# Optimization experiments

Measured on AMD Instinct MI355X. Metric: run time of the kernel, lower is better.

The kernel has to match this reference:

```python
import jax, jax.numpy as jnp
import numpy as np

N = 50000          # nodes
E = 800000         # edges per metapath
P = 4              # metapaths
IN = 256           # in_size
D = 32 * 8         # out_size * layer_num_heads = 256
SEM_H = 128        # SemanticAttention hidden


def setup_inputs() -> dict:
    key = jax.random.key(0)
    ks = jax.random.split(key, 8)
    h = jax.random.normal(ks[0], (N, IN), dtype=jnp.float32)
    src = jax.random.randint(ks[1], (P, E), 0, N, dtype=jnp.int32)
    dst = jax.random.randint(ks[2], (P, E), 0, N, dtype=jnp.int32)
    # per-metapath GraphConv weights (Glorot-ish scale)
    W_gc = jax.random.normal(ks[3], (P, IN, D), dtype=jnp.float32) / np.sqrt(IN)
    b_gc = jnp.zeros((P, D), dtype=jnp.float32)
    # SemanticAttention: Linear(D, SEM_H) -> tanh -> Linear(SEM_H, 1, bias=False)
    W1 = jax.random.normal(ks[4], (D, SEM_H), dtype=jnp.float32) / np.sqrt(D)
    b1 = jnp.zeros((SEM_H,), dtype=jnp.float32)
    w2 = jax.random.normal(ks[5], (SEM_H,), dtype=jnp.float32) / np.sqrt(SEM_H)
    return {"h": h, "src": src, "dst": dst, "W_gc": W_gc, "b_gc": b_gc,
            "W1": W1, "b1": b1, "w2": w2}


def _graph_conv(h, src, dst, W, b):
    # DGL GraphConv with norm='both': D_dst^{-1/2} A D_src^{-1/2} (h W) + b
    ones = jnp.ones((src.shape[0],), dtype=h.dtype)
    deg_out = jnp.clip(jax.ops.segment_sum(ones, src, num_segments=N), 1.0)
    deg_in = jnp.clip(jax.ops.segment_sum(ones, dst, num_segments=N), 1.0)
    x = (h @ W) * jax.lax.rsqrt(deg_out)[:, None]          # [N, D]
    agg = jax.ops.segment_sum(x[src], dst, num_segments=N)  # gather-scatter [N, D]
    return agg * jax.lax.rsqrt(deg_in)[:, None] + b


def reference(h, src, dst, W_gc, b_gc, W1, b1, w2):
    # per-metapath GraphConv (fixed small loop over P metapaths)
    zs = [_graph_conv(h, src[p], dst[p], W_gc[p], b_gc[p]) for p in range(P)]
    z = jnp.stack(zs, axis=1)                               # [N, P, D]
    # SemanticAttention: project -> mean over nodes -> softmax over metapaths
    s = jnp.tanh(z @ W1 + b1) @ w2                          # [N, P]
    beta = jax.nn.softmax(s.mean(axis=0), axis=0)           # [P]
    return jnp.einsum('npd,p->nd', z, beta)                 # [N, D]
```

## Files before the change

### kernel.cpp

```cpp
#include <hip/hip_runtime.h>

#define NN 50000
#define NE 800000
#define NP 4
#define DIN 256
#define DD 256
#define NH 128
#define SA 40
#define NSEG 16
#define SEGE (NE / NSEG)
#define HCH 16384
#define NHC 4
#define SCH 8192
#define NSC 7
#define SPAD(k) ((k) + ((k) >> 5))

typedef __attribute__((ext_vector_type(8))) short bf16x8;
typedef __attribute__((ext_vector_type(4))) float f32x4;
typedef __attribute__((ext_vector_type(2))) float f32x2;

__device__ __forceinline__ unsigned short f2bf(float f) {
  unsigned u = __float_as_uint(f);
  u += 0x7fff + ((u >> 16) & 1);
  return (unsigned short)(u >> 16);
}
__device__ __forceinline__ float bfl(unsigned u) { return __uint_as_float(u << 16); }
__device__ __forceinline__ float bfh(unsigned u) { return __uint_as_float(u & 0xffff0000u); }


__global__ __launch_bounds__(256) void hist2d_kernel(const int* __restrict__ idx,
                                                     int* __restrict__ cnt) {
  int bx = blockIdx.x;
  int c = bx % NHC, s = bx / NHC;
  int p = blockIdx.y;
  int base = c * HCH, nk = min(HCH, NN - base);
  __shared__ int hs[HCH];
  for (int k = threadIdx.x; k < HCH; k += 256) hs[k] = 0;
  __syncthreads();
  const int4* a4 = (const int4*)(idx + (size_t)p * NE + (size_t)s * SEGE);
  for (int i = threadIdx.x; i < SEGE / 4; i += 256) {
    int4 v = a4[i];
    int k;
    k = v.x - base; if ((unsigned)k < (unsigned)nk) atomicAdd(&hs[k], 1);
    k = v.y - base; if ((unsigned)k < (unsigned)nk) atomicAdd(&hs[k], 1);
    k = v.z - base; if ((unsigned)k < (unsigned)nk) atomicAdd(&hs[k], 1);
    k = v.w - base; if ((unsigned)k < (unsigned)nk) atomicAdd(&hs[k], 1);
  }
  __syncthreads();
  int* out = cnt + (size_t)(p * NSEG + s) * NN + base;
  for (int k = threadIdx.x; k < nk; k += 256) out[k] = hs[k];
}


__global__ __launch_bounds__(1024) void scanA_kernel(
    int* __restrict__ cntD, const int* __restrict__ cntS,
    float* __restrict__ rin, float* __restrict__ rout,
    int* __restrict__ row_ptr, int* __restrict__ chunkdeg) {
  int c = blockIdx.x, p = blockIdx.y;
  int base = c * SCH, nk = min(SCH, NN - base);
  __shared__ int sdeg[SCH + (SCH >> 5)];
  __shared__ int wtot[16], wexc[16];
  int t = threadIdx.x;
  for (int kk = t; kk < SCH; kk += 1024) {
    int run = 0;
    if (kk < nk) {
      size_t o = (size_t)(p * NSEG) * NN + base + kk;
      for (int s = 0; s < NSEG; ++s) {
        size_t oo = o + (size_t)s * NN;
        int v = cntD[oo];
        cntD[oo] = run;
        run += v;
      }
      rin[(size_t)p * NN + base + kk] = rsqrtf((float)max(run, 1));
      int rs = 0;
      for (int s = 0; s < NSEG; ++s) rs += cntS[o + (size_t)s * NN];
      rout[(size_t)p * NN + base + kk] = rsqrtf((float)max(rs, 1));
    }
    sdeg[SPAD(kk)] = run;
  }
  __syncthreads();
  int loc[8];
  int ssum = 0;
#pragma unroll
  for (int j = 0; j < 8; ++j) { loc[j] = ssum; ssum += sdeg[SPAD(t * 8 + j)]; }
  int incl = ssum;
  int lane = t & 63, w = t >> 6;
#pragma unroll
  for (int o = 1; o < 64; o <<= 1) {
    int v = __shfl_up(incl, o);
    if (lane >= o) incl += v;
  }
  if (lane == 63) wtot[w] = incl;
  __syncthreads();
  if (t == 0) {
    int r = 0;
    for (int i = 0; i < 16; ++i) { wexc[i] = r; r += wtot[i]; }
  }
  __syncthreads();
  int tbase = wexc[w] + incl - ssum;
  int* rp = row_ptr + (size_t)p * (NN + 1) + base;
#pragma unroll
  for (int j = 0; j < 8; ++j) {
    int k = t * 8 + j;
    if (k < nk) rp[k] = tbase + loc[j];
  }
  if (t == 1023) chunkdeg[p * NSC + c] = tbase + ssum;
}


__global__ void scanB_kernel(const int* __restrict__ chunkdeg, int* __restrict__ chunk_base,
                             int* __restrict__ row_ptr) {
  int t = threadIdx.x;
  if (t < NP) {
    int run = 0;
    for (int c = 0; c < NSC; ++c) { chunk_base[t * NSC + c] = run; run += chunkdeg[t * NSC + c]; }
    row_ptr[(size_t)t * (NN + 1) + NN] = NE;
  }
}

__global__ __launch_bounds__(1024) void rpfin_kernel(int* __restrict__ row_ptr,
                                                     const int* __restrict__ chunk_base) {
  int k = blockIdx.x * 1024 + threadIdx.x, p = blockIdx.y;
  if (k < NN) row_ptr[(size_t)p * (NN + 1) + k] += chunk_base[p * NSC + (k >> 13)];
}


__global__ __launch_bounds__(256) void scatter_kernel(
    const int* __restrict__ src, const int* __restrict__ dst,
    const int* __restrict__ cntD, const int* __restrict__ row_ptr, int* __restrict__ col) {
  int bx = blockIdx.x;
  int c = bx % NHC, s = bx / NHC;
  int p = blockIdx.y;
  int base = c * HCH, nk = min(HCH, NN - base);
  __shared__ int cur[HCH];
  for (int k = threadIdx.x; k < nk; k += 256)
    cur[k] = row_ptr[(size_t)p * (NN + 1) + base + k] +
             cntD[(size_t)(p * NSEG + s) * NN + base + k];
  __syncthreads();
  const int4* d4 = (const int4*)(dst + (size_t)p * NE + (size_t)s * SEGE);
  const int4* s4 = (const int4*)(src + (size_t)p * NE + (size_t)s * SEGE);
  int* colp = col + (size_t)p * NE;
  for (int i = threadIdx.x; i < SEGE / 4; i += 256) {
    int4 dv = d4[i];
    int4 sv = s4[i];
    int k;
    k = dv.x - base; if ((unsigned)k < (unsigned)nk) colp[atomicAdd(&cur[k], 1)] = sv.x;
    k = dv.y - base; if ((unsigned)k < (unsigned)nk) colp[atomicAdd(&cur[k], 1)] = sv.y;
    k = dv.z - base; if ((unsigned)k < (unsigned)nk) colp[atomicAdd(&cur[k], 1)] = sv.z;
    k = dv.w - base; if ((unsigned)k < (unsigned)nk) colp[atomicAdd(&cur[k], 1)] = sv.w;
  }
}


__global__ void cvt_h_kernel(const float4* __restrict__ h4, ushort4* __restrict__ h2) {
  int i = blockIdx.x * blockDim.x + threadIdx.x;
  if (i >= NN * DIN / 4) return;
  float4 v = h4[i];
  ushort4 o;
  o.x = f2bf(v.x); o.y = f2bf(v.y); o.z = f2bf(v.z); o.w = f2bf(v.w);
  h2[i] = o;
}


__global__ __launch_bounds__(256) void agg_kernel(
    const ushort* __restrict__ h2, const int* __restrict__ col,
    const int* __restrict__ row_ptr, const float* __restrict__ rout,
    const float* __restrict__ rin, ushort* __restrict__ g) {
  __shared__ int2 sW[4][64];
  int p = blockIdx.y;
  int v = blockIdx.x * 4 + (threadIdx.x >> 6);
  int lane = threadIdx.x & 63;
  int wv = threadIdx.x >> 6;
  const int* colp = col + (size_t)p * NE;
  const float* rop = rout + (size_t)p * NN;
  int beg = row_ptr[p * (NN + 1) + v], end = row_ptr[p * (NN + 1) + v + 1];
  const char* hb = (const char*)h2 + (size_t)lane * 8;
  f32x2 accA0 = {0.f, 0.f}, accA1 = {0.f, 0.f};
  f32x2 accB0 = {0.f, 0.f}, accB1 = {0.f, 0.f};
  for (int j0 = beg; j0 < end; j0 += 64) {
    int nw = end - j0;
    if (nw > 64) nw = 64;
    int cv = 0;
    float rv = 0.f;
    if (lane < nw) { cv = colp[j0 + lane]; rv = rop[cv]; }
    sW[wv][lane] = make_int2(cv, __float_as_int(rv));
    int nwb = (nw + 7) & ~7;
    for (int t = 0; t < nwb; t += 8) {
      int2 w[8];
#pragma unroll
      for (int q = 0; q < 8; ++q) w[q] = sW[wv][t + q];
      uint2 u[8];
#pragma unroll
      for (int q = 0; q < 8; ++q)
        u[q] = *(const uint2*)(hb + ((size_t)(unsigned)w[q].x << 9));
#pragma unroll
      for (int q = 0; q < 8; ++q) {
        float r = __int_as_float(w[q].y);
        f32x2 rr = {r, r};
        if (q & 1) {
          asm("v_pk_fma_f32 %0, %1, %2, %0" : "+v"(accB0) : "v"(rr), "v"((f32x2){bfl(u[q].x), bfh(u[q].x)}));
          asm("v_pk_fma_f32 %0, %1, %2, %0" : "+v"(accB1) : "v"(rr), "v"((f32x2){bfl(u[q].y), bfh(u[q].y)}));
        } else {
          asm("v_pk_fma_f32 %0, %1, %2, %0" : "+v"(accA0) : "v"(rr), "v"((f32x2){bfl(u[q].x), bfh(u[q].x)}));
          asm("v_pk_fma_f32 %0, %1, %2, %0" : "+v"(accA1) : "v"(rr), "v"((f32x2){bfl(u[q].y), bfh(u[q].y)}));
        }
      }
    }
  }
  float ri = rin[(size_t)p * NN + v];
  f32x2 s0 = accA0 + accB0;
  f32x2 s1 = accA1 + accB1;
  ushort4 o;
  o.x = f2bf(s0.x * ri); o.y = f2bf(s0.y * ri);
  o.z = f2bf(s1.x * ri); o.w = f2bf(s1.y * ri);
  ((ushort4*)(g + ((size_t)p * NN + v) * DIN))[lane] = o;
}


__global__ void wmulcvec_kernel(const float* __restrict__ Wgc, const float* __restrict__ bgc,
                                const float* __restrict__ W1, const float* __restrict__ b1,
                                ushort* __restrict__ Mt, float* __restrict__ cvec) {
  int p = blockIdx.y, k = blockIdx.x, j = threadIdx.x;
  if (k < DIN) {
    const float* wrow = Wgc + ((size_t)p * DIN + k) * DD;
    float s = 0.f;
    for (int d = 0; d < DD; ++d) s = fmaf(wrow[d], W1[(size_t)d * NH + j], s);
    Mt[((size_t)p * NH + j) * DIN + k] = f2bf(s);
  } else {
    const float* b = bgc + (size_t)p * DD;
    float s = b1[j];
    for (int d = 0; d < DD; ++d) s = fmaf(b[d], W1[(size_t)d * NH + j], s);
    cvec[p * NH + j] = s;
  }
}


__global__ __launch_bounds__(256) void gemm_sem(
    const ushort* __restrict__ g, const ushort* __restrict__ Mt,
    const float* __restrict__ cvec, const float* __restrict__ w2,
    float* __restrict__ ssum) {
  __shared__ ushort As[128 * SA];
  __shared__ ushort Bs[128 * SA];
  __shared__ float wsumf[4];
  const int tid = threadIdx.x;
  const int p = blockIdx.y;
  const int row0 = blockIdx.x * 128;
  const int wave = tid >> 6, lane = tid & 63;
  const int wr = wave >> 1, wc = wave & 1;
  const int srow = tid >> 2, sseg = tid & 3;
  const int fr = lane & 15, fk = (lane >> 4) * 8;
  const ushort* Ag = g + (size_t)p * NN * DIN;
  const ushort* Bg = Mt + (size_t)p * NH * DIN;
  int ar0 = row0 + srow; if (ar0 >= NN) ar0 = NN - 1;
  int ar1 = row0 + srow + 64; if (ar1 >= NN) ar1 = NN - 1;
  f32x4 acc[4][4] = {};
  for (int k2 = 0; k2 < DIN; k2 += 32) {
    uint4 av0 = *(const uint4*)(Ag + (size_t)ar0 * DIN + k2 + sseg * 8);
    uint4 av1 = *(const uint4*)(Ag + (size_t)ar1 * DIN + k2 + sseg * 8);
    uint4 bv0 = *(const uint4*)(Bg + (size_t)srow * DIN + k2 + sseg * 8);
    uint4 bv1 = *(const uint4*)(Bg + (size_t)(srow + 64) * DIN + k2 + sseg * 8);
    __syncthreads();
    *(uint4*)&As[srow * SA + sseg * 8] = av0;
    *(uint4*)&As[(srow + 64) * SA + sseg * 8] = av1;
    *(uint4*)&Bs[srow * SA + sseg * 8] = bv0;
    *(uint4*)&Bs[(srow + 64) * SA + sseg * 8] = bv1;
    __syncthreads();
    bf16x8 af[4], bfv[4];
#pragma unroll
    for (int t = 0; t < 4; ++t) {
      af[t] = *(const bf16x8*)&As[(wr * 64 + t * 16 + fr) * SA + fk];
      bfv[t] = *(const bf16x8*)&Bs[(wc * 64 + t * 16 + fr) * SA + fk];
    }
#pragma unroll
    for (int mt = 0; mt < 4; ++mt)
#pragma unroll
      for (int nt = 0; nt < 4; ++nt)
        acc[mt][nt] = __builtin_amdgcn_mfma_f32_16x16x32_bf16(af[mt], bfv[nt], acc[mt][nt], 0, 0, 0);
  }
  float s = 0.f;
#pragma unroll
  for (int nt = 0; nt < 4; ++nt) {
    int c = wc * 64 + nt * 16 + fr;
    float cc = cvec[p * NH + c];
    float ww = w2[c];
#pragma unroll
    for (int mt = 0; mt < 4; ++mt)
#pragma unroll
      for (int i = 0; i < 4; ++i) {
        int r = row0 + wr * 64 + mt * 16 + (lane >> 4) * 4 + i;
        if (r < NN) {
          float x = acc[mt][nt][i] + cc;
          x = fminf(fmaxf(x, -15.f), 15.f);
          float e = __expf(2.f * x);
          s = fmaf((e - 1.f) / (e + 1.f), ww, s);
        }
      }
  }
#pragma unroll
  for (int o = 32; o > 0; o >>= 1) s += __shfl_down(s, o);
  if (lane == 0) wsumf[wave] = s;
  __syncthreads();
  if (tid == 0) atomicAdd(&ssum[p], wsumf[0] + wsumf[1] + wsumf[2] + wsumf[3]);
}


__global__ __launch_bounds__(256) void scaleWtB_kernel(const float* __restrict__ Wgc,
                                                       const float* __restrict__ ssum,
                                                       const float* __restrict__ bgc,
                                                       ushort* __restrict__ Wt,
                                                       float* __restrict__ bout) {
  float m[NP];
  float mx = -1e30f;
#pragma unroll
  for (int p = 0; p < NP; ++p) {
    m[p] = ssum[p] * (1.f / (float)NN);
    mx = fmaxf(mx, m[p]);
  }
  float tot = 0.f;
#pragma unroll
  for (int p = 0; p < NP; ++p) { m[p] = __expf(m[p] - mx); tot += m[p]; }
  float inv = 1.f / tot;
  if (blockIdx.x == 0) {
    int d = threadIdx.x;
    float s = 0.f;
#pragma unroll
    for (int p = 0; p < NP; ++p) s = fmaf(m[p] * inv, bgc[p * DD + d], s);
    bout[d] = s;
  }
  int i = blockIdx.x * 256 + threadIdx.x;
  if (i < DD * NP * DIN) {
    int n = i >> 10;
    int pk = i & 1023;
    int p = pk >> 8, k = pk & 255;
    Wt[i] = f2bf(m[p] * inv * Wgc[((size_t)p * DIN + k) * DD + n]);
  }
}


__global__ __launch_bounds__(256) void gemm_main(
    const ushort* __restrict__ g, const ushort* __restrict__ Wt,
    const float* __restrict__ bout, float* __restrict__ out) {
  __shared__ ushort As[128 * SA];
  __shared__ ushort Bs[256 * SA];
  const int tid = threadIdx.x;
  const int row0 = blockIdx.x * 128;
  const int wave = tid >> 6, lane = tid & 63;
  const int wr = wave >> 1, wc = wave & 1;
  const int srow = tid >> 2, sseg = tid & 3;
  const int fr = lane & 15, fk = (lane >> 4) * 8;
  int ar0 = row0 + srow; if (ar0 >= NN) ar0 = NN - 1;
  int ar1 = row0 + srow + 64; if (ar1 >= NN) ar1 = NN - 1;
  f32x4 acc[4][8] = {};
  for (int p = 0; p < NP; ++p) {
    const ushort* Ag = g + (size_t)p * NN * DIN;
    for (int k2 = 0; k2 < DIN; k2 += 32) {
      uint4 av0 = *(const uint4*)(Ag + (size_t)ar0 * DIN + k2 + sseg * 8);
      uint4 av1 = *(const uint4*)(Ag + (size_t)ar1 * DIN + k2 + sseg * 8);
      uint4 bv0 = *(const uint4*)(Wt + (size_t)srow * (NP * DIN) + p * DIN + k2 + sseg * 8);
      uint4 bv1 = *(const uint4*)(Wt + (size_t)(srow + 64) * (NP * DIN) + p * DIN + k2 + sseg * 8);
      uint4 bv2 = *(const uint4*)(Wt + (size_t)(srow + 128) * (NP * DIN) + p * DIN + k2 + sseg * 8);
      uint4 bv3 = *(const uint4*)(Wt + (size_t)(srow + 192) * (NP * DIN) + p * DIN + k2 + sseg * 8);
      __syncthreads();
      *(uint4*)&As[srow * SA + sseg * 8] = av0;
      *(uint4*)&As[(srow + 64) * SA + sseg * 8] = av1;
      *(uint4*)&Bs[srow * SA + sseg * 8] = bv0;
      *(uint4*)&Bs[(srow + 64) * SA + sseg * 8] = bv1;
      *(uint4*)&Bs[(srow + 128) * SA + sseg * 8] = bv2;
      *(uint4*)&Bs[(srow + 192) * SA + sseg * 8] = bv3;
      __syncthreads();
      bf16x8 af[4], bfv[8];
#pragma unroll
      for (int t = 0; t < 4; ++t)
        af[t] = *(const bf16x8*)&As[(wr * 64 + t * 16 + fr) * SA + fk];
#pragma unroll
      for (int nt = 0; nt < 8; ++nt)
        bfv[nt] = *(const bf16x8*)&Bs[(wc * 128 + nt * 16 + fr) * SA + fk];
#pragma unroll
      for (int mt = 0; mt < 4; ++mt)
#pragma unroll
        for (int nt = 0; nt < 8; ++nt)
          acc[mt][nt] = __builtin_amdgcn_mfma_f32_16x16x32_bf16(af[mt], bfv[nt], acc[mt][nt], 0, 0, 0);
    }
  }
#pragma unroll
  for (int nt = 0; nt < 8; ++nt) {
    int c = wc * 128 + nt * 16 + fr;
    float bb = bout[c];
#pragma unroll
    for (int mt = 0; mt < 4; ++mt)
#pragma unroll
      for (int i = 0; i < 4; ++i) {
        int r = row0 + wr * 64 + mt * 16 + (lane >> 4) * 4 + i;
        if (r < NN) out[(size_t)r * DD + c] = acc[mt][nt][i] + bb;
      }
  }
}


extern "C" void kernel_launch(void* const* d_in, const int* in_sizes, int n_in,
                              void* d_out, int out_size, void* d_ws, size_t ws_size,
                              hipStream_t stream) {
  const float* h = (const float*)d_in[0];
  const int* src = (const int*)d_in[1];
  const int* dst = (const int*)d_in[2];
  const float* Wgc = (const float*)d_in[3];
  const float* bgc = (const float*)d_in[4];
  const float* W1 = (const float*)d_in[5];
  const float* b1 = (const float*)d_in[6];
  const float* w2 = (const float*)d_in[7];
  float* out = (float*)d_out;

  char* base = (char*)d_ws;
  size_t off = 0;
  auto alloc = [&](size_t bytes) -> char* {
    char* ptr = base + off;
    off = (off + bytes + 255) & ~(size_t)255;
    return ptr;
  };
  int* cntD = (int*)alloc((size_t)NP * NSEG * NN * sizeof(int));
  int* cntS = (int*)alloc((size_t)NP * NSEG * NN * sizeof(int));
  float* rin = (float*)alloc((size_t)NP * NN * sizeof(float));
  float* rout = (float*)alloc((size_t)NP * NN * sizeof(float));
  int* row_ptr = (int*)alloc((size_t)NP * (NN + 1) * sizeof(int));
  int* chunkdeg = (int*)alloc((size_t)NP * NSC * sizeof(int));
  int* chunk_base = (int*)alloc((size_t)NP * NSC * sizeof(int));
  ushort* h2 = (ushort*)alloc((size_t)NN * DIN * sizeof(ushort));
  ushort* g = (ushort*)alloc((size_t)NP * NN * DIN * sizeof(ushort));
  ushort* Mt = (ushort*)alloc((size_t)NP * NH * DIN * sizeof(ushort));
  ushort* Wt = (ushort*)alloc((size_t)DD * NP * DIN * sizeof(ushort));
  float* cvec = (float*)alloc((size_t)NP * NH * sizeof(float));
  float* ssum = (float*)alloc(NP * sizeof(float));
  float* bout = (float*)alloc(DD * sizeof(float));
  int* colbuf = (int*)cntS;
  if (off > ws_size) return;

  hipMemsetAsync(ssum, 0, NP * sizeof(float), stream);

  hist2d_kernel<<<dim3(NHC * NSEG, NP), 256, 0, stream>>>(dst, cntD);
  hist2d_kernel<<<dim3(NHC * NSEG, NP), 256, 0, stream>>>(src, cntS);
  scanA_kernel<<<dim3(NSC, NP), 1024, 0, stream>>>(cntD, cntS, rin, rout, row_ptr, chunkdeg);
  scanB_kernel<<<1, 64, 0, stream>>>(chunkdeg, chunk_base, row_ptr);
  rpfin_kernel<<<dim3((NN + 1023) / 1024, NP), 1024, 0, stream>>>(row_ptr, chunk_base);
  cvt_h_kernel<<<(NN * DIN / 4 + 255) / 256, 256, 0, stream>>>((const float4*)h, (ushort4*)h2);
  scatter_kernel<<<dim3(NHC * NSEG, NP), 256, 0, stream>>>(src, dst, cntD, row_ptr, colbuf);
  agg_kernel<<<dim3(NN / 4, NP), 256, 0, stream>>>(h2, colbuf, row_ptr, rout, rin, g);
  wmulcvec_kernel<<<dim3(DIN + 1, NP), NH, 0, stream>>>(Wgc, bgc, W1, b1, Mt, cvec);
  gemm_sem<<<dim3((NN + 127) / 128, NP), 256, 0, stream>>>(g, Mt, cvec, w2, ssum);
  scaleWtB_kernel<<<(DD * NP * DIN + 255) / 256, 256, 0, stream>>>(Wgc, ssum, bgc, Wt, bout);
  gemm_main<<<dim3((NN + 127) / 128), 256, 0, stream>>>(g, Wt, bout, out);
}
```

Before: 635.1 us.

## Merge histogram launches, shrink counts to ushort, fold scanB into rpfin

The two histogram kernels become one launch that picks src or dst through blockIdx.z. The per-segment count arrays shrink from int to ushort to cut their memory traffic, and the histogram and scatter chunks grow to 32K shared-memory entries with half as many chunk passes over the edges. The tiny scanB kernel is removed: each rpfin thread sums the chunk degrees itself and also writes the row_ptr terminator. colbuf gets its own buffer instead of aliasing cntS. The larger shared arrays (128 KB) may reduce occupancy, and ushort counts rely on per-segment counts staying below 65536.

```diff
diff --git a/kernel.cpp b/kernel.cpp
--- a/kernel.cpp
+++ b/kernel.cpp
@@ -9,8 +9,8 @@
 #define SA 40
 #define NSEG 16
 #define SEGE (NE / NSEG)
-#define HCH 16384
-#define NHC 4
+#define HCH 32768
+#define NHC 2
 #define SCH 8192
 #define NSC 7
 #define SPAD(k) ((k) + ((k) >> 5))
@@ -28,13 +28,17 @@
 __device__ __forceinline__ float bfh(unsigned u) { return __uint_as_float(u & 0xffff0000u); }
 
 
-__global__ __launch_bounds__(256) void hist2d_kernel(const int* __restrict__ idx,
-                                                     int* __restrict__ cnt) {
+__global__ __launch_bounds__(256) void histX_kernel(const int* __restrict__ src,
+                                                    const int* __restrict__ dst,
+                                                    ushort* __restrict__ cntS,
+                                                    ushort* __restrict__ cntD) {
+  __shared__ int hs[HCH];
   int bx = blockIdx.x;
   int c = bx % NHC, s = bx / NHC;
   int p = blockIdx.y;
+  const int* idx = blockIdx.z ? dst : src;
+  ushort* cnt = blockIdx.z ? cntD : cntS;
   int base = c * HCH, nk = min(HCH, NN - base);
-  __shared__ int hs[HCH];
   for (int k = threadIdx.x; k < HCH; k += 256) hs[k] = 0;
   __syncthreads();
   const int4* a4 = (const int4*)(idx + (size_t)p * NE + (size_t)s * SEGE);
@@ -47,13 +51,13 @@
     k = v.w - base; if ((unsigned)k < (unsigned)nk) atomicAdd(&hs[k], 1);
   }
   __syncthreads();
-  int* out = cnt + (size_t)(p * NSEG + s) * NN + base;
-  for (int k = threadIdx.x; k < nk; k += 256) out[k] = hs[k];
+  ushort* out = cnt + (size_t)(p * NSEG + s) * NN + base;
+  for (int k = threadIdx.x; k < nk; k += 256) out[k] = (ushort)hs[k];
 }
 
 
 __global__ __launch_bounds__(1024) void scanA_kernel(
-    int* __restrict__ cntD, const int* __restrict__ cntS,
+    ushort* __restrict__ cntD, const ushort* __restrict__ cntS,
     float* __restrict__ rin, float* __restrict__ rout,
     int* __restrict__ row_ptr, int* __restrict__ chunkdeg) {
   int c = blockIdx.x, p = blockIdx.y;
@@ -65,14 +69,16 @@
     int run = 0;
     if (kk < nk) {
       size_t o = (size_t)(p * NSEG) * NN + base + kk;
+#pragma unroll
       for (int s = 0; s < NSEG; ++s) {
         size_t oo = o + (size_t)s * NN;
         int v = cntD[oo];
-        cntD[oo] = run;
+        cntD[oo] = (ushort)run;
         run += v;
       }
       rin[(size_t)p * NN + base + kk] = rsqrtf((float)max(run, 1));
       int rs = 0;
+#pragma unroll
       for (int s = 0; s < NSEG; ++s) rs += cntS[o + (size_t)s * NN];
       rout[(size_t)p * NN + base + kk] = rsqrtf((float)max(rs, 1));
     }
@@ -108,31 +114,27 @@
 }
 
 
-__global__ void scanB_kernel(const int* __restrict__ chunkdeg, int* __restrict__ chunk_base,
-                             int* __restrict__ row_ptr) {
-  int t = threadIdx.x;
-  if (t < NP) {
-    int run = 0;
-    for (int c = 0; c < NSC; ++c) { chunk_base[t * NSC + c] = run; run += chunkdeg[t * NSC + c]; }
-    row_ptr[(size_t)t * (NN + 1) + NN] = NE;
-  }
-}
-
 __global__ __launch_bounds__(1024) void rpfin_kernel(int* __restrict__ row_ptr,
-                                                     const int* __restrict__ chunk_base) {
+                                                     const int* __restrict__ chunkdeg) {
   int k = blockIdx.x * 1024 + threadIdx.x, p = blockIdx.y;
-  if (k < NN) row_ptr[(size_t)p * (NN + 1) + k] += chunk_base[p * NSC + (k >> 13)];
+  if (k < NN) {
+    int c = k >> 13;
+    int cb = 0;
+    for (int i = 0; i < c; ++i) cb += chunkdeg[p * NSC + i];
+    row_ptr[(size_t)p * (NN + 1) + k] += cb;
+  }
+  if (k == 0) row_ptr[(size_t)p * (NN + 1) + NN] = NE;
 }
 
 
 __global__ __launch_bounds__(256) void scatter_kernel(
     const int* __restrict__ src, const int* __restrict__ dst,
-    const int* __restrict__ cntD, const int* __restrict__ row_ptr, int* __restrict__ col) {
+    const ushort* __restrict__ cntD, const int* __restrict__ row_ptr, int* __restrict__ col) {
+  __shared__ int cur[HCH];
   int bx = blockIdx.x;
   int c = bx % NHC, s = bx / NHC;
   int p = blockIdx.y;
   int base = c * HCH, nk = min(HCH, NN - base);
-  __shared__ int cur[HCH];
   for (int k = threadIdx.x; k < nk; k += 256)
     cur[k] = row_ptr[(size_t)p * (NN + 1) + base + k] +
              cntD[(size_t)(p * NSEG + s) * NN + base + k];
@@ -417,13 +419,13 @@
     off = (off + bytes + 255) & ~(size_t)255;
     return ptr;
   };
-  int* cntD = (int*)alloc((size_t)NP * NSEG * NN * sizeof(int));
-  int* cntS = (int*)alloc((size_t)NP * NSEG * NN * sizeof(int));
+  ushort* cntD = (ushort*)alloc((size_t)NP * NSEG * NN * sizeof(ushort));
+  ushort* cntS = (ushort*)alloc((size_t)NP * NSEG * NN * sizeof(ushort));
   float* rin = (float*)alloc((size_t)NP * NN * sizeof(float));
   float* rout = (float*)alloc((size_t)NP * NN * sizeof(float));
   int* row_ptr = (int*)alloc((size_t)NP * (NN + 1) * sizeof(int));
   int* chunkdeg = (int*)alloc((size_t)NP * NSC * sizeof(int));
-  int* chunk_base = (int*)alloc((size_t)NP * NSC * sizeof(int));
+  int* colbuf = (int*)alloc((size_t)NP * NE * sizeof(int));
   ushort* h2 = (ushort*)alloc((size_t)NN * DIN * sizeof(ushort));
   ushort* g = (ushort*)alloc((size_t)NP * NN * DIN * sizeof(ushort));
   ushort* Mt = (ushort*)alloc((size_t)NP * NH * DIN * sizeof(ushort));
@@ -431,16 +433,13 @@
   float* cvec = (float*)alloc((size_t)NP * NH * sizeof(float));
   float* ssum = (float*)alloc(NP * sizeof(float));
   float* bout = (float*)alloc(DD * sizeof(float));
-  int* colbuf = (int*)cntS;
   if (off > ws_size) return;
 
   hipMemsetAsync(ssum, 0, NP * sizeof(float), stream);
 
-  hist2d_kernel<<<dim3(NHC * NSEG, NP), 256, 0, stream>>>(dst, cntD);
-  hist2d_kernel<<<dim3(NHC * NSEG, NP), 256, 0, stream>>>(src, cntS);
+  histX_kernel<<<dim3(NHC * NSEG, NP, 2), 256, 0, stream>>>(src, dst, cntS, cntD);
   scanA_kernel<<<dim3(NSC, NP), 1024, 0, stream>>>(cntD, cntS, rin, rout, row_ptr, chunkdeg);
-  scanB_kernel<<<1, 64, 0, stream>>>(chunkdeg, chunk_base, row_ptr);
-  rpfin_kernel<<<dim3((NN + 1023) / 1024, NP), 1024, 0, stream>>>(row_ptr, chunk_base);
+  rpfin_kernel<<<dim3((NN + 1023) / 1024, NP), 1024, 0, stream>>>(row_ptr, chunkdeg);
   cvt_h_kernel<<<(NN * DIN / 4 + 255) / 256, 256, 0, stream>>>((const float4*)h, (ushort4*)h2);
   scatter_kernel<<<dim3(NHC * NSEG, NP), 256, 0, stream>>>(src, dst, cntD, row_ptr, colbuf);
   agg_kernel<<<dim3(NN / 4, NP), 256, 0, stream>>>(h2, colbuf, row_ptr, rout, rin, g);
```

Result: faster. 593.6 us (-6.5%).
